# Optimization experiments

Hardware: AMD Instinct MI355X
Metric: run time of the kernel (lower is better)

Reference implementation:

```python
import jax, jax.numpy as jnp
import numpy as np

HIDDEN = 1024
MEM = 50
MAX_POS = 200
BATCH, SEQ = 256, 200


def setup_inputs() -> dict:
    key = jax.random.key(0)
    ks = jax.random.split(key, 5)
    x = jax.random.normal(ks[0], (BATCH, SEQ, HIDDEN), dtype=jnp.float32)
    spatial_memory = jax.random.normal(ks[1], (MEM, HIDDEN), dtype=jnp.float32)
    pos_encoding = jax.random.normal(ks[2], (1, MAX_POS, HIDDEN), dtype=jnp.float32)
    # nn.Linear(2H, H): weight [H, 2H], bias [H]
    bound = 1.0 / np.sqrt(2 * HIDDEN)
    gate_w = jax.random.uniform(ks[3], (HIDDEN, 2 * HIDDEN), jnp.float32, -bound, bound)
    gate_b = jax.random.uniform(ks[4], (HIDDEN,), jnp.float32, -bound, bound)
    return {"x": x, "spatial_memory": spatial_memory, "pos_encoding": pos_encoding,
            "gate_w": gate_w, "gate_b": gate_b}


def reference(x, spatial_memory, pos_encoding, gate_w, gate_b):
    seq_len = x.shape[1]
    # add position encoding (sliced to seq_len)
    feats = x + pos_encoding[:, :seq_len, :]                      # [B,S,H]
    # cross-attention over small fixed memory bank
    sim = jnp.einsum('bsh,mh->bsm', feats, spatial_memory)        # [B,S,M]
    w = jax.nn.softmax(sim, axis=-1)
    mem_read = jnp.einsum('bsm,mh->bsh', w, spatial_memory)       # [B,S,H]
    # gated update: sigmoid(Linear(concat)) -- split weight to avoid concat
    w_f, w_m = gate_w[:, :HIDDEN], gate_w[:, HIDDEN:]
    gate = jax.nn.sigmoid(jnp.einsum('bsh,oh->bso', feats, w_f)
                          + jnp.einsum('bsh,oh->bso', mem_read, w_m)
                          + gate_b)
    return feats + gate * mem_read
```

## Files before the change

kernel.cpp:

```cpp
#include <hip/hip_runtime.h>
#include <cstdint>
#include <cstddef>

#define HD   1024
#define SEQL 200
#define MEMN 50
#define RTOT 51200
#define KP   128
#define PADK 136

typedef float  f4    __attribute__((ext_vector_type(4)));
typedef float  f32x4 __attribute__((ext_vector_type(4)));
typedef short  s16x8 __attribute__((ext_vector_type(8)));
typedef unsigned short u16;
typedef unsigned short u16x4 __attribute__((ext_vector_type(4)));
typedef unsigned short u16x8 __attribute__((ext_vector_type(8)));

__device__ __forceinline__ u16 f2bf(float f) {
    unsigned u = __builtin_bit_cast(unsigned, f);
    u += 0x7FFFu + ((u >> 16) & 1u);
    return (u16)(u >> 16);
}
__device__ __forceinline__ float bf2f(u16 h) {
    unsigned u = ((unsigned)h) << 16;
    return __builtin_bit_cast(float, u);
}

#define GLOAD_LDS16(g, l) __builtin_amdgcn_global_load_lds( \
    (const __attribute__((address_space(1))) unsigned int*)(g), \
    (__attribute__((address_space(3))) unsigned int*)(l), 16, 0, 0)

#define WAITV3 asm volatile("s_waitcnt vmcnt(3)" ::: "memory")
#define WAITV0 asm volatile("s_waitcnt vmcnt(0)" ::: "memory")
#define LGKMFENCE asm volatile("s_waitcnt lgkmcnt(0)" ::: "memory")
#define SCHB   __builtin_amdgcn_sched_barrier(0)

__global__ __launch_bounds__(256) void k_cvt_w(const float* __restrict__ gw,
                                               u16* __restrict__ gwB)
{
    const size_t i = ((size_t)blockIdx.x * 256 + threadIdx.x) * 8;
    f4 v0 = *(const f4*)&gw[i];
    f4 v1 = *(const f4*)&gw[i + 4];
    u16x4 b0 = { f2bf(v0.x), f2bf(v0.y), f2bf(v0.z), f2bf(v0.w) };
    u16x4 b1 = { f2bf(v1.x), f2bf(v1.y), f2bf(v1.z), f2bf(v1.w) };
    *(u16x4*)&gwB[i]     = b0;
    *(u16x4*)&gwB[i + 4] = b1;
}

__global__ __launch_bounds__(256) void k_prep_mem(const float* __restrict__ sm,
                                                  u16* __restrict__ memHi,
                                                  u16* __restrict__ memLo,
                                                  u16* __restrict__ memT)
{
    const int idx = blockIdx.x * 256 + threadIdx.x;
    const int m  = idx >> 8;
    const int h0 = (idx & 255) * 4;
    f4 v = {0.f, 0.f, 0.f, 0.f};
    if (m < MEMN) v = *(const f4*)&sm[(size_t)m * HD + h0];
    u16x4 hi = { f2bf(v.x), f2bf(v.y), f2bf(v.z), f2bf(v.w) };
    f4 hv = { bf2f(hi.x), bf2f(hi.y), bf2f(hi.z), bf2f(hi.w) };
    f4 lv = v - hv;
    u16x4 lo = { f2bf(lv.x), f2bf(lv.y), f2bf(lv.z), f2bf(lv.w) };
    *(u16x4*)&memHi[(size_t)m * HD + h0] = hi;
    *(u16x4*)&memLo[(size_t)m * HD + h0] = lo;
    memT[(size_t)(h0 + 0) * 64 + m] = hi.x;
    memT[(size_t)(h0 + 1) * 64 + m] = hi.y;
    memT[(size_t)(h0 + 2) * 64 + m] = hi.z;
    memT[(size_t)(h0 + 3) * 64 + m] = hi.w;
}

__global__ __launch_bounds__(256) void k_mwm(const u16* __restrict__ memHi,
                                             const u16* __restrict__ gwB,
                                             u16* __restrict__ MWmT)
{
    const int tid = threadIdx.x, lane = tid & 63, w = tid >> 6;
    const int fr = lane & 15, fk = (lane >> 4) * 8, jr = (lane >> 4) * 4;
    const int ob = blockIdx.x * 64 + w * 16;
    f32x4 acc[4] = {};
    for (int ks = 0; ks < 32; ++ks) {
        s16x8 b = *(const s16x8*)&gwB[(size_t)(ob + fr) * 2048 + 1024 + ks * 32 + fk];
        #pragma unroll
        for (int mt = 0; mt < 4; ++mt) {
            s16x8 a = *(const s16x8*)&memHi[(size_t)(mt * 16 + fr) * HD + ks * 32 + fk];
            acc[mt] = __builtin_amdgcn_mfma_f32_16x16x32_bf16(a, b, acc[mt], 0, 0, 0);
        }
    }
    #pragma unroll
    for (int mt = 0; mt < 4; ++mt)
        #pragma unroll
        for (int j = 0; j < 4; ++j)
            MWmT[(size_t)(ob + fr) * 64 + mt * 16 + jr + j] = f2bf(acc[mt][j]);
}

__global__ __launch_bounds__(256) void k_pre(
    const float* __restrict__ x, const float* __restrict__ pos,
    const u16* __restrict__ memHi, const u16* __restrict__ memLo,
    u16* __restrict__ featsB, u16* __restrict__ wBg)
{
    __shared__ u16 fHi[64 * PADK];
    __shared__ u16 fLo[64 * PADK];

    const int tid  = threadIdx.x;
    const int r0   = blockIdx.x * 64;
    const int lane = tid & 63, w = tid >> 6;
    const int fr   = lane & 15;
    const int fk   = (lane >> 4) * 8;
    const int jr   = (lane >> 4) * 4;

    const int srow = tid >> 2;
    const int scol = (tid & 3) * 8;
    const int prow = (r0 + srow) % SEQL;

    const float* xrow = &x[(size_t)(r0 + srow) * HD];
    const float* prp  = &pos[(size_t)prow * HD];

    f4 xa[4][2], pa[4][2];
    #pragma unroll
    for (int i = 0; i < 4; ++i) {
        const int c = scol + i * 32;
        xa[i][0] = *(const f4*)&xrow[c];
        xa[i][1] = *(const f4*)&xrow[c + 4];
        pa[i][0] = *(const f4*)&prp[c];
        pa[i][1] = *(const f4*)&prp[c + 4];
    }

    f32x4 acc[4] = {};

    for (int kp = 0; kp < HD; kp += KP) {
        #pragma unroll
        for (int i = 0; i < 4; ++i) {
            const int c = scol + i * 32;
            f4 fa = xa[i][0] + pa[i][0];
            f4 fb = xa[i][1] + pa[i][1];
            u16x8 hi = { f2bf(fa.x), f2bf(fa.y), f2bf(fa.z), f2bf(fa.w),
                         f2bf(fb.x), f2bf(fb.y), f2bf(fb.z), f2bf(fb.w) };
            *(u16x8*)&featsB[(size_t)(r0 + srow) * HD + kp + c] = hi;
            f4 hv0 = { bf2f(hi[0]), bf2f(hi[1]), bf2f(hi[2]), bf2f(hi[3]) };
            f4 hv1 = { bf2f(hi[4]), bf2f(hi[5]), bf2f(hi[6]), bf2f(hi[7]) };
            f4 l0 = fa - hv0, l1 = fb - hv1;
            u16x8 lo = { f2bf(l0.x), f2bf(l0.y), f2bf(l0.z), f2bf(l0.w),
                         f2bf(l1.x), f2bf(l1.y), f2bf(l1.z), f2bf(l1.w) };
            *(u16x8*)&fHi[srow * PADK + c] = hi;
            *(u16x8*)&fLo[srow * PADK + c] = lo;
        }
        LGKMFENCE;

        if (kp + KP < HD) {
            #pragma unroll
            for (int i = 0; i < 4; ++i) {
                const int c = kp + KP + scol + i * 32;
                xa[i][0] = *(const f4*)&xrow[c];
                xa[i][1] = *(const f4*)&xrow[c + 4];
                pa[i][0] = *(const f4*)&prp[c];
                pa[i][1] = *(const f4*)&prp[c + 4];
            }
        }

        #pragma unroll
        for (int ks = 0; ks < KP / 32; ++ks) {
            const int kb = ks * 32 + fk;
            s16x8 aH = *(const s16x8*)&fHi[(16 * w + fr) * PADK + kb];
            s16x8 aL = *(const s16x8*)&fLo[(16 * w + fr) * PADK + kb];
            #pragma unroll
            for (int n = 0; n < 4; ++n) {
                const size_t mb = (size_t)(n * 16 + fr) * HD + kp + kb;
                s16x8 bH = *(const s16x8*)&memHi[mb];
                s16x8 bL = *(const s16x8*)&memLo[mb];
                acc[n] = __builtin_amdgcn_mfma_f32_16x16x32_bf16(aH, bH, acc[n], 0, 0, 0);
                acc[n] = __builtin_amdgcn_mfma_f32_16x16x32_bf16(aH, bL, acc[n], 0, 0, 0);
                acc[n] = __builtin_amdgcn_mfma_f32_16x16x32_bf16(aL, bH, acc[n], 0, 0, 0);
            }
        }
        LGKMFENCE;
    }

    #pragma unroll
    for (int j = 0; j < 4; ++j) {
        const int rg = r0 + 16 * w + jr + j;
        float v[4];
        float mx = -1e30f;
        #pragma unroll
        for (int n = 0; n < 4; ++n) {
            v[n] = acc[n][j];
            const int m = n * 16 + fr;
            if (m < MEMN) mx = fmaxf(mx, v[n]);
        }
        #pragma unroll
        for (int d = 1; d < 16; d <<= 1) mx = fmaxf(mx, __shfl_xor(mx, d));
        float e[4], s = 0.f;
        #pragma unroll
        for (int n = 0; n < 4; ++n) {
            const int m = n * 16 + fr;
            e[n] = (m < MEMN) ? __expf(v[n] - mx) : 0.f;
            s += e[n];
        }
        #pragma unroll
        for (int d = 1; d < 16; d <<= 1) s += __shfl_xor(s, d);
        const float inv = 1.f / s;
        #pragma unroll
        for (int n = 0; n < 4; ++n)
            wBg[(size_t)rg * 64 + n * 16 + fr] = f2bf(e[n] * inv);
    }
}

__global__ __launch_bounds__(512) void k_gate_out(
    const u16* __restrict__ featsB, const u16* __restrict__ wBg,
    const u16* __restrict__ gwB, const u16* __restrict__ memT,
    const u16* __restrict__ MWmT, const float* __restrict__ gb,
    float* __restrict__ out)
{
    __shared__ u16 As[2][256 * 32];
    __shared__ u16 Bs[2][128 * 32];

    const int tid = threadIdx.x;
    int bid = blockIdx.x;
    bid = (bid & 7) * 200 + (bid >> 3);
    const int mt = bid >> 3, nt = bid & 7;
    const int row0 = mt * 256, col0 = nt * 128;
    const int lane = tid & 63, wave = tid >> 6;
    const int wm = wave >> 1, wn = wave & 1;
    const int fr = lane & 15, fk = (lane >> 4) * 8;

    f32x4 acc[4][4] = {};

    const int sr = tid >> 2;
    const int sc = (tid & 3) * 8;

    auto stage = [&](int buf, int kt) {
        if (kt < 32) {
            const int k0 = kt * 32;
            GLOAD_LDS16(featsB + (size_t)(row0 + sr) * HD + k0 + sc,       &As[buf][tid * 8]);
            GLOAD_LDS16(featsB + (size_t)(row0 + 128 + sr) * HD + k0 + sc, &As[buf][4096 + tid * 8]);
            GLOAD_LDS16(gwB + (size_t)(col0 + sr) * 2048 + k0 + sc,        &Bs[buf][tid * 8]);
        } else {
            const int k0 = (kt - 32) * 32;
            GLOAD_LDS16(wBg + (size_t)(row0 + sr) * 64 + k0 + sc,          &As[buf][tid * 8]);
            GLOAD_LDS16(wBg + (size_t)(row0 + 128 + sr) * 64 + k0 + sc,    &As[buf][4096 + tid * 8]);
            GLOAD_LDS16(MWmT + (size_t)(col0 + sr) * 64 + k0 + sc,         &Bs[buf][tid * 8]);
        }
    };

    stage(0, 0);
    int cur = 0;

    for (int kt = 0; kt < 34; ++kt) {
        if (kt < 33) {
            stage(cur ^ 1, kt + 1);
            WAITV3;
        } else {
            WAITV0;
        }
        __builtin_amdgcn_s_barrier();
        SCHB;

        s16x8 aF[4], bF[4];
        #pragma unroll
        for (int m = 0; m < 4; ++m)
            aF[m] = *(const s16x8*)&As[cur][(wm * 64 + m * 16 + fr) * 32 + fk];
        #pragma unroll
        for (int n = 0; n < 4; ++n)
            bF[n] = *(const s16x8*)&Bs[cur][(wn * 64 + n * 16 + fr) * 32 + fk];
        #pragma unroll
        for (int m = 0; m < 4; ++m)
            #pragma unroll
            for (int n = 0; n < 4; ++n)
                acc[m][n] = __builtin_amdgcn_mfma_f32_16x16x32_bf16(
                    aF[m], bF[n], acc[m][n], 0, 0, 0);

        SCHB;
        __builtin_amdgcn_s_barrier();
        cur ^= 1;
    }

    #pragma unroll
    for (int m = 0; m < 4; ++m) {
        const size_t ab = (size_t)(row0 + wm * 64 + m * 16 + fr) * 64 + fk;
        s16x8 a2_0 = *(const s16x8*)&wBg[ab];
        s16x8 a2_1 = *(const s16x8*)&wBg[ab + 32];
        #pragma unroll
        for (int n = 0; n < 4; ++n) {
            const size_t cb = (size_t)(col0 + wn * 64 + n * 16 + fr) * 64 + fk;
            s16x8 bT0 = *(const s16x8*)&memT[cb];
            s16x8 bT1 = *(const s16x8*)&memT[cb + 32];
            f32x4 accR = {};
            accR = __builtin_amdgcn_mfma_f32_16x16x32_bf16(a2_0, bT0, accR, 0, 0, 0);
            accR = __builtin_amdgcn_mfma_f32_16x16x32_bf16(a2_1, bT1, accR, 0, 0, 0);

            const int crow = row0 + wm * 64 + m * 16 + (lane >> 4) * 4;
            const int ccol = col0 + wn * 64 + n * 16 + fr;
            const float bias = gb[ccol];
            #pragma unroll
            for (int j = 0; j < 4; ++j) {
                const size_t idx = (size_t)(crow + j) * HD + ccol;
                const float fe = bf2f(featsB[idx]);
                const float pre = acc[m][n][j] + bias;
                const float g = 1.0f / (1.0f + __expf(-pre));
                out[idx] = fe + g * accR[j];
            }
        }
    }
}

extern "C" void kernel_launch(void* const* d_in, const int* in_sizes, int n_in,
                              void* d_out, int out_size, void* d_ws, size_t ws_size,
                              hipStream_t stream)
{
    const float* x   = (const float*)d_in[0];
    const float* sm  = (const float*)d_in[1];
    const float* pos = (const float*)d_in[2];
    const float* gw  = (const float*)d_in[3];
    const float* gb  = (const float*)d_in[4];
    float* out = (float*)d_out;

    u16* featsB = (u16*)d_ws;
    u16* gwB    = featsB + (size_t)RTOT * HD;
    u16* wBg    = gwB + (size_t)HD * 2048;
    u16* memHi  = wBg + (size_t)RTOT * 64;
    u16* memLo  = memHi + 64 * HD;
    u16* memT   = memLo + 64 * HD;
    u16* MWmT   = memT + (size_t)HD * 64;

    k_cvt_w<<<dim3(1024), dim3(256), 0, stream>>>(gw, gwB);
    k_prep_mem<<<dim3(64), dim3(256), 0, stream>>>(sm, memHi, memLo, memT);
    k_mwm<<<dim3(16), dim3(256), 0, stream>>>(memHi, gwB, MWmT);
    k_pre<<<dim3(RTOT / 64), dim3(256), 0, stream>>>(x, pos, memHi, memLo,
                                                     featsB, wBg);
    k_gate_out<<<dim3(1600), dim3(512), 0, stream>>>(featsB, wBg, gwB, memT,
                                                     MWmT, gb, out);
}
```

Measured before the change: 441.8 us.

## Triple-buffer gate GEMM with BK=64, XOR-swizzled LDS, and split-phase staging

Restructures the main gate GEMM loop: K tile doubles from 32 to 64, LDS goes from double to triple buffering, and staging is split into two chunks interleaved with the two MFMA phases of each tile. LDS rows are XOR-swizzled to avoid bank conflicts on fragment reads, and s_setprio raises wave priority around the MFMA blocks. The aim is deeper prefetch and fewer barriers per K step so global loads hide better behind compute. It raises LDS use to about 144KB per block, and together with the launch_bounds min-blocks hint of 2 this may limit occupancy.

```diff
diff --git a/kernel.cpp b/kernel.cpp
--- a/kernel.cpp
+++ b/kernel.cpp
@@ -30,7 +30,7 @@
     (const __attribute__((address_space(1))) unsigned int*)(g), \
     (__attribute__((address_space(3))) unsigned int*)(l), 16, 0, 0)
 
-#define WAITV3 asm volatile("s_waitcnt vmcnt(3)" ::: "memory")
+#define WAITV6 asm volatile("s_waitcnt vmcnt(6)" ::: "memory")
 #define WAITV0 asm volatile("s_waitcnt vmcnt(0)" ::: "memory")
 #define LGKMFENCE asm volatile("s_waitcnt lgkmcnt(0)" ::: "memory")
 #define SCHB   __builtin_amdgcn_sched_barrier(0)
@@ -203,14 +203,14 @@
     }
 }
 
-__global__ __launch_bounds__(512) void k_gate_out(
+__global__ __launch_bounds__(512, 2) void k_gate_out(
     const u16* __restrict__ featsB, const u16* __restrict__ wBg,
     const u16* __restrict__ gwB, const u16* __restrict__ memT,
     const u16* __restrict__ MWmT, const float* __restrict__ gb,
     float* __restrict__ out)
 {
-    __shared__ u16 As[2][256 * 32];
-    __shared__ u16 Bs[2][128 * 32];
+    __shared__ u16 As[3][256 * 64];
+    __shared__ u16 Bs[3][128 * 64];
 
     const int tid = threadIdx.x;
     int bid = blockIdx.x;
@@ -219,57 +219,83 @@
     const int row0 = mt * 256, col0 = nt * 128;
     const int lane = tid & 63, wave = tid >> 6;
     const int wm = wave >> 1, wn = wave & 1;
-    const int fr = lane & 15, fk = (lane >> 4) * 8;
+    const int fr = lane & 15, sg = lane >> 4;
+    const int fk = sg * 8;
 
     f32x4 acc[4][4] = {};
 
-    const int sr = tid >> 2;
-    const int sc = (tid & 3) * 8;
-
-    auto stage = [&](int buf, int kt) {
-        if (kt < 32) {
-            const int k0 = kt * 32;
-            GLOAD_LDS16(featsB + (size_t)(row0 + sr) * HD + k0 + sc,       &As[buf][tid * 8]);
-            GLOAD_LDS16(featsB + (size_t)(row0 + 128 + sr) * HD + k0 + sc, &As[buf][4096 + tid * 8]);
-            GLOAD_LDS16(gwB + (size_t)(col0 + sr) * 2048 + k0 + sc,        &Bs[buf][tid * 8]);
+    const int rr = tid >> 3;
+    const int sl = tid & 7;
+
+    auto stageChunk = [&](int buf, int kt, int c) {
+        if (kt < 16) {
+            const int k0 = kt * 64;
+            const int ra0 = c * 128 + rr;
+            GLOAD_LDS16(featsB + (size_t)(row0 + ra0) * HD + k0 + ((sl ^ (ra0 & 7)) * 8),
+                        &As[buf][(c * 128) * 64 + tid * 8]);
+            const int ra1 = c * 128 + 64 + rr;
+            GLOAD_LDS16(featsB + (size_t)(row0 + ra1) * HD + k0 + ((sl ^ (ra1 & 7)) * 8),
+                        &As[buf][(c * 128 + 64) * 64 + tid * 8]);
+            const int rb = c * 64 + rr;
+            GLOAD_LDS16(gwB + (size_t)(col0 + rb) * 2048 + k0 + ((sl ^ (rb & 7)) * 8),
+                        &Bs[buf][(c * 64) * 64 + tid * 8]);
         } else {
-            const int k0 = (kt - 32) * 32;
-            GLOAD_LDS16(wBg + (size_t)(row0 + sr) * 64 + k0 + sc,          &As[buf][tid * 8]);
-            GLOAD_LDS16(wBg + (size_t)(row0 + 128 + sr) * 64 + k0 + sc,    &As[buf][4096 + tid * 8]);
-            GLOAD_LDS16(MWmT + (size_t)(col0 + sr) * 64 + k0 + sc,         &Bs[buf][tid * 8]);
+            const int ra0 = c * 128 + rr;
+            GLOAD_LDS16(wBg + (size_t)(row0 + ra0) * 64 + ((sl ^ (ra0 & 7)) * 8),
+                        &As[buf][(c * 128) * 64 + tid * 8]);
+            const int ra1 = c * 128 + 64 + rr;
+            GLOAD_LDS16(wBg + (size_t)(row0 + ra1) * 64 + ((sl ^ (ra1 & 7)) * 8),
+                        &As[buf][(c * 128 + 64) * 64 + tid * 8]);
+            const int rb = c * 64 + rr;
+            GLOAD_LDS16(MWmT + (size_t)(col0 + rb) * 64 + ((sl ^ (rb & 7)) * 8),
+                        &Bs[buf][(c * 64) * 64 + tid * 8]);
         }
     };
 
-    stage(0, 0);
-    int cur = 0;
-
-    for (int kt = 0; kt < 34; ++kt) {
-        if (kt < 33) {
-            stage(cur ^ 1, kt + 1);
-            WAITV3;
-        } else {
-            WAITV0;
-        }
-        __builtin_amdgcn_s_barrier();
-        SCHB;
-
-        s16x8 aF[4], bF[4];
-        #pragma unroll
-        for (int m = 0; m < 4; ++m)
-            aF[m] = *(const s16x8*)&As[cur][(wm * 64 + m * 16 + fr) * 32 + fk];
-        #pragma unroll
-        for (int n = 0; n < 4; ++n)
-            bF[n] = *(const s16x8*)&Bs[cur][(wn * 64 + n * 16 + fr) * 32 + fk];
-        #pragma unroll
-        for (int m = 0; m < 4; ++m)
-            #pragma unroll
-            for (int n = 0; n < 4; ++n)
-                acc[m][n] = __builtin_amdgcn_mfma_f32_16x16x32_bf16(
-                    aF[m], bF[n], acc[m][n], 0, 0, 0);
-
-        SCHB;
-        __builtin_amdgcn_s_barrier();
-        cur ^= 1;
+    stageChunk(0, 0, 0); stageChunk(0, 0, 1);
+    stageChunk(1, 1, 0); stageChunk(1, 1, 1);
+    WAITV6;
+    __builtin_amdgcn_s_barrier();
+
+    s16x8 aF[4], bF[4];
+
+    for (int T = 0; T < 17; ++T) {
+        const int buf = T % 3;
+        const int nbuf = (T + 2) % 3;
+        const bool doStage = (T + 2 <= 16);
+
+        #pragma unroll
+        for (int ph = 0; ph < 2; ++ph) {
+            #pragma unroll
+            for (int i = 0; i < 4; ++i) {
+                const int r = wm * 64 + i * 16 + fr;
+                const int s = (ph * 4 + sg) ^ (fr & 7);
+                aF[i] = *(const s16x8*)&As[buf][r * 64 + s * 8];
+            }
+            #pragma unroll
+            for (int n = 0; n < 4; ++n) {
+                const int r = wn * 64 + n * 16 + fr;
+                const int s = (ph * 4 + sg) ^ (fr & 7);
+                bF[n] = *(const s16x8*)&Bs[buf][r * 64 + s * 8];
+            }
+            if (doStage) stageChunk(nbuf, T + 2, ph);
+            if (ph == 1) {
+                if (T <= 14)      WAITV6;
+                else if (T == 15) WAITV0;
+            }
+            __builtin_amdgcn_s_barrier();
+            LGKMFENCE;
+            SCHB;
+            __builtin_amdgcn_s_setprio(1);
+            #pragma unroll
+            for (int i = 0; i < 4; ++i)
+                #pragma unroll
+                for (int n = 0; n < 4; ++n)
+                    acc[i][n] = __builtin_amdgcn_mfma_f32_16x16x32_bf16(
+                        aF[i], bF[n], acc[i][n], 0, 0, 0);
+            __builtin_amdgcn_s_setprio(0);
+            __builtin_amdgcn_s_barrier();
+        }
     }
 
     #pragma unroll
@@ -286,7 +312,7 @@
             accR = __builtin_amdgcn_mfma_f32_16x16x32_bf16(a2_0, bT0, accR, 0, 0, 0);
             accR = __builtin_amdgcn_mfma_f32_16x16x32_bf16(a2_1, bT1, accR, 0, 0, 0);
 
-            const int crow = row0 + wm * 64 + m * 16 + (lane >> 4) * 4;
+            const int crow = row0 + wm * 64 + m * 16 + sg * 4;
             const int ccol = col0 + wn * 64 + n * 16 + fr;
             const float bias = gb[ccol];
             #pragma unroll
```

New measurement: 444.0 us. Within noise of the previous version (+0.5%).

## Split feature conversion from similarity kernel and stage bf16 tiles via async LDS loads

Applied to the files above, without the earlier changes.

Moves the x+pos add and the bf16 hi/lo split into a separate streaming kernel that writes featsB and a lo-part buffer (placed in the output buffer as scratch). The similarity kernel then double-buffers those bf16 tiles into XOR-swizzled shared memory with global_load_lds and waitcnt fencing, instead of converting in registers with lgkm fences. The aim is to overlap loads with the MFMA work and remove the serialized conversion in the sim loop. The cost is an extra round trip through global memory for the lo buffer (about 100MB written and read back) plus one more kernel launch.

```diff
diff --git a/kernel.cpp b/kernel.cpp
--- a/kernel.cpp
+++ b/kernel.cpp
@@ -6,8 +6,6 @@
 #define SEQL 200
 #define MEMN 50
 #define RTOT 51200
-#define KP   128
-#define PADK 136
 
 typedef float  f4    __attribute__((ext_vector_type(4)));
 typedef float  f32x4 __attribute__((ext_vector_type(4)));
@@ -30,9 +28,9 @@
     (const __attribute__((address_space(1))) unsigned int*)(g), \
     (__attribute__((address_space(3))) unsigned int*)(l), 16, 0, 0)
 
+#define WAITV4 asm volatile("s_waitcnt vmcnt(4)" ::: "memory")
 #define WAITV3 asm volatile("s_waitcnt vmcnt(3)" ::: "memory")
 #define WAITV0 asm volatile("s_waitcnt vmcnt(0)" ::: "memory")
-#define LGKMFENCE asm volatile("s_waitcnt lgkmcnt(0)" ::: "memory")
 #define SCHB   __builtin_amdgcn_sched_barrier(0)
 
 __global__ __launch_bounds__(256) void k_cvt_w(const float* __restrict__ gw,
@@ -92,78 +90,80 @@
             MWmT[(size_t)(ob + fr) * 64 + mt * 16 + jr + j] = f2bf(acc[mt][j]);
 }
 
-__global__ __launch_bounds__(256) void k_pre(
-    const float* __restrict__ x, const float* __restrict__ pos,
+__global__ __launch_bounds__(256) void k_feats(const float* __restrict__ x,
+                                               const float* __restrict__ pos,
+                                               u16* __restrict__ featsB,
+                                               u16* __restrict__ featsLo)
+{
+    const size_t stride = (size_t)gridDim.x * 256 * 8;
+    for (size_t e = ((size_t)blockIdx.x * 256 + threadIdx.x) * 8;
+         e < (size_t)RTOT * HD; e += stride) {
+        const int row  = (int)(e >> 10);
+        const int col  = (int)(e & 1023);
+        const int prow = row % SEQL;
+        f4 x0 = *(const f4*)&x[e];
+        f4 x1 = *(const f4*)&x[e + 4];
+        f4 p0 = *(const f4*)&pos[(size_t)prow * HD + col];
+        f4 p1 = *(const f4*)&pos[(size_t)prow * HD + col + 4];
+        f4 fa = x0 + p0, fb = x1 + p1;
+        u16x8 hi = { f2bf(fa.x), f2bf(fa.y), f2bf(fa.z), f2bf(fa.w),
+                     f2bf(fb.x), f2bf(fb.y), f2bf(fb.z), f2bf(fb.w) };
+        f4 hv0 = { bf2f(hi[0]), bf2f(hi[1]), bf2f(hi[2]), bf2f(hi[3]) };
+        f4 hv1 = { bf2f(hi[4]), bf2f(hi[5]), bf2f(hi[6]), bf2f(hi[7]) };
+        f4 l0 = fa - hv0, l1 = fb - hv1;
+        u16x8 lo = { f2bf(l0.x), f2bf(l0.y), f2bf(l0.z), f2bf(l0.w),
+                     f2bf(l1.x), f2bf(l1.y), f2bf(l1.z), f2bf(l1.w) };
+        *(u16x8*)&featsB[e]  = hi;
+        *(u16x8*)&featsLo[e] = lo;
+    }
+}
+
+__global__ __launch_bounds__(256) void k_sim(
+    const u16* __restrict__ featsB, const u16* __restrict__ featsLo,
     const u16* __restrict__ memHi, const u16* __restrict__ memLo,
-    u16* __restrict__ featsB, u16* __restrict__ wBg)
-{
-    __shared__ u16 fHi[64 * PADK];
-    __shared__ u16 fLo[64 * PADK];
+    u16* __restrict__ wBg)
+{
+    __shared__ u16 S[2][4][2][1024];
 
     const int tid  = threadIdx.x;
+    const int lane = tid & 63, w = tid >> 6;
+    const int fr   = lane & 15, sg = lane >> 4;
+    const int fk   = sg * 8, jr = sg * 4;
     const int r0   = blockIdx.x * 64;
-    const int lane = tid & 63, w = tid >> 6;
-    const int fr   = lane & 15;
-    const int fk   = (lane >> 4) * 8;
-    const int jr   = (lane >> 4) * 4;
-
-    const int srow = tid >> 2;
-    const int scol = (tid & 3) * 8;
-    const int prow = (r0 + srow) % SEQL;
-
-    const float* xrow = &x[(size_t)(r0 + srow) * HD];
-    const float* prp  = &pos[(size_t)prow * HD];
-
-    f4 xa[4][2], pa[4][2];
-    #pragma unroll
-    for (int i = 0; i < 4; ++i) {
-        const int c = scol + i * 32;
-        xa[i][0] = *(const f4*)&xrow[c];
-        xa[i][1] = *(const f4*)&xrow[c + 4];
-        pa[i][0] = *(const f4*)&prp[c];
-        pa[i][1] = *(const f4*)&prp[c + 4];
-    }
+    const int rowbase = r0 + 16 * w;
+
+    const int lrow = lane >> 3;
+    const int lslot = lane & 7;
+    const int srcsl = (lslot ^ lrow) * 8;
+
+    auto stage = [&](int b, int p) {
+        #pragma unroll
+        for (int g = 0; g < 2; ++g) {
+            const int r = rowbase + g * 8 + lrow;
+            GLOAD_LDS16(featsB  + (size_t)r * HD + p * 64 + srcsl,
+                        &S[b][w][0][g * 512]);
+            GLOAD_LDS16(featsLo + (size_t)r * HD + p * 64 + srcsl,
+                        &S[b][w][1][g * 512]);
+        }
+    };
 
     f32x4 acc[4] = {};
 
-    for (int kp = 0; kp < HD; kp += KP) {
-        #pragma unroll
-        for (int i = 0; i < 4; ++i) {
-            const int c = scol + i * 32;
-            f4 fa = xa[i][0] + pa[i][0];
-            f4 fb = xa[i][1] + pa[i][1];
-            u16x8 hi = { f2bf(fa.x), f2bf(fa.y), f2bf(fa.z), f2bf(fa.w),
-                         f2bf(fb.x), f2bf(fb.y), f2bf(fb.z), f2bf(fb.w) };
-            *(u16x8*)&featsB[(size_t)(r0 + srow) * HD + kp + c] = hi;
-            f4 hv0 = { bf2f(hi[0]), bf2f(hi[1]), bf2f(hi[2]), bf2f(hi[3]) };
-            f4 hv1 = { bf2f(hi[4]), bf2f(hi[5]), bf2f(hi[6]), bf2f(hi[7]) };
-            f4 l0 = fa - hv0, l1 = fb - hv1;
-            u16x8 lo = { f2bf(l0.x), f2bf(l0.y), f2bf(l0.z), f2bf(l0.w),
-                         f2bf(l1.x), f2bf(l1.y), f2bf(l1.z), f2bf(l1.w) };
-            *(u16x8*)&fHi[srow * PADK + c] = hi;
-            *(u16x8*)&fLo[srow * PADK + c] = lo;
-        }
-        LGKMFENCE;
-
-        if (kp + KP < HD) {
-            #pragma unroll
-            for (int i = 0; i < 4; ++i) {
-                const int c = kp + KP + scol + i * 32;
-                xa[i][0] = *(const f4*)&xrow[c];
-                xa[i][1] = *(const f4*)&xrow[c + 4];
-                pa[i][0] = *(const f4*)&prp[c];
-                pa[i][1] = *(const f4*)&prp[c + 4];
-            }
-        }
-
-        #pragma unroll
-        for (int ks = 0; ks < KP / 32; ++ks) {
-            const int kb = ks * 32 + fk;
-            s16x8 aH = *(const s16x8*)&fHi[(16 * w + fr) * PADK + kb];
-            s16x8 aL = *(const s16x8*)&fLo[(16 * w + fr) * PADK + kb];
+    stage(0, 0);
+    for (int p = 0; p < 16; ++p) {
+        const int b = p & 1;
+        if (p < 15) { stage(b ^ 1, p + 1); WAITV4; }
+        else        { WAITV0; }
+        SCHB;
+
+        #pragma unroll
+        for (int ks = 0; ks < 2; ++ks) {
+            const int sl = ((ks * 4 + sg) ^ (fr & 7)) * 8;
+            s16x8 aH = *(const s16x8*)&S[b][w][0][fr * 64 + sl];
+            s16x8 aL = *(const s16x8*)&S[b][w][1][fr * 64 + sl];
             #pragma unroll
             for (int n = 0; n < 4; ++n) {
-                const size_t mb = (size_t)(n * 16 + fr) * HD + kp + kb;
+                const size_t mb = (size_t)(n * 16 + fr) * HD + p * 64 + ks * 32 + fk;
                 s16x8 bH = *(const s16x8*)&memHi[mb];
                 s16x8 bL = *(const s16x8*)&memLo[mb];
                 acc[n] = __builtin_amdgcn_mfma_f32_16x16x32_bf16(aH, bH, acc[n], 0, 0, 0);
@@ -171,7 +171,6 @@
                 acc[n] = __builtin_amdgcn_mfma_f32_16x16x32_bf16(aL, bH, acc[n], 0, 0, 0);
             }
         }
-        LGKMFENCE;
     }
 
     #pragma unroll
@@ -320,11 +319,14 @@
     u16* memT   = memLo + 64 * HD;
     u16* MWmT   = memT + (size_t)HD * 64;
 
+    u16* featsLo = (u16*)d_out;
+
     k_cvt_w<<<dim3(1024), dim3(256), 0, stream>>>(gw, gwB);
     k_prep_mem<<<dim3(64), dim3(256), 0, stream>>>(sm, memHi, memLo, memT);
     k_mwm<<<dim3(16), dim3(256), 0, stream>>>(memHi, gwB, MWmT);
-    k_pre<<<dim3(RTOT / 64), dim3(256), 0, stream>>>(x, pos, memHi, memLo,
-                                                     featsB, wBg);
+    k_feats<<<dim3(1600), dim3(256), 0, stream>>>(x, pos, featsB, featsLo);
+    k_sim<<<dim3(RTOT / 64), dim3(256), 0, stream>>>(featsB, featsLo,
+                                                     memHi, memLo, wBg);
     k_gate_out<<<dim3(1600), dim3(512), 0, stream>>>(featsB, wBg, gwB, memT,
                                                      MWmT, gb, out);
 }
```

After: 471.5 us. +6.7%, slower.

## Stage swizzled memory bank through LDS with double-buffered async loads in k_pre

Applied to the files above, without the earlier changes.

Rather than having every wave read the hi/lo memory-bank operands straight from global memory, k_prep_mem now writes them in an XOR-swizzled, panel-major layout. k_pre then copies 64-column panels into double-buffered LDS through direct global-to-LDS loads, overlapped with the feature conversion. The K panel shrinks from 128 to 64 columns, and a workgroup barrier is added each step. The aim is to cut redundant global/L2 traffic and bank conflicts, at the cost of more LDS use and an extra barrier per step. The reuse of a fLo/fHi and memory buffer across iterations relies on that barrier ordering, so a read-write race is a risk.

```diff
diff --git a/kernel.cpp b/kernel.cpp
--- a/kernel.cpp
+++ b/kernel.cpp
@@ -6,8 +6,7 @@
 #define SEQL 200
 #define MEMN 50
 #define RTOT 51200
-#define KP   128
-#define PADK 136
+#define PK   72
 
 typedef float  f4    __attribute__((ext_vector_type(4)));
 typedef float  f32x4 __attribute__((ext_vector_type(4)));
@@ -49,8 +48,9 @@
 
 __global__ __launch_bounds__(256) void k_prep_mem(const float* __restrict__ sm,
                                                   u16* __restrict__ memHi,
-                                                  u16* __restrict__ memLo,
-                                                  u16* __restrict__ memT)
+                                                  u16* __restrict__ memT,
+                                                  u16* __restrict__ memSH,
+                                                  u16* __restrict__ memSL)
 {
     const int idx = blockIdx.x * 256 + threadIdx.x;
     const int m  = idx >> 8;
@@ -62,11 +62,14 @@
     f4 lv = v - hv;
     u16x4 lo = { f2bf(lv.x), f2bf(lv.y), f2bf(lv.z), f2bf(lv.w) };
     *(u16x4*)&memHi[(size_t)m * HD + h0] = hi;
-    *(u16x4*)&memLo[(size_t)m * HD + h0] = lo;
     memT[(size_t)(h0 + 0) * 64 + m] = hi.x;
     memT[(size_t)(h0 + 1) * 64 + m] = hi.y;
     memT[(size_t)(h0 + 2) * 64 + m] = hi.z;
     memT[(size_t)(h0 + 3) * 64 + m] = hi.w;
+    const int p = h0 >> 6, s = (h0 >> 3) & 7, e = h0 & 7;
+    const size_t sw = (size_t)p * 4096 + m * 64 + ((s ^ (m & 7)) << 3) + e;
+    *(u16x4*)&memSH[sw] = hi;
+    *(u16x4*)&memSL[sw] = lo;
 }
 
 __global__ __launch_bounds__(256) void k_mwm(const u16* __restrict__ memHi,
@@ -94,84 +97,98 @@
 
 __global__ __launch_bounds__(256) void k_pre(
     const float* __restrict__ x, const float* __restrict__ pos,
-    const u16* __restrict__ memHi, const u16* __restrict__ memLo,
+    const u16* __restrict__ memSH, const u16* __restrict__ memSL,
     u16* __restrict__ featsB, u16* __restrict__ wBg)
 {
-    __shared__ u16 fHi[64 * PADK];
-    __shared__ u16 fLo[64 * PADK];
+    __shared__ u16 fHi[64 * PK];
+    __shared__ u16 fLo[64 * PK];
+    __shared__ u16 memH[2][64 * 64];
+    __shared__ u16 memL[2][64 * 64];
 
     const int tid  = threadIdx.x;
     const int r0   = blockIdx.x * 64;
     const int lane = tid & 63, w = tid >> 6;
-    const int fr   = lane & 15;
-    const int fk   = (lane >> 4) * 8;
-    const int jr   = (lane >> 4) * 4;
+    const int fr   = lane & 15, sg = lane >> 4;
+    const int fk   = sg * 8, jr = sg * 4;
 
     const int srow = tid >> 2;
-    const int scol = (tid & 3) * 8;
+    const int scol = (tid & 3) * 16;
     const int prow = (r0 + srow) % SEQL;
-
     const float* xrow = &x[(size_t)(r0 + srow) * HD];
     const float* prp  = &pos[(size_t)prow * HD];
 
-    f4 xa[4][2], pa[4][2];
+    f4 xa[4], pa[4];
     #pragma unroll
     for (int i = 0; i < 4; ++i) {
-        const int c = scol + i * 32;
-        xa[i][0] = *(const f4*)&xrow[c];
-        xa[i][1] = *(const f4*)&xrow[c + 4];
-        pa[i][0] = *(const f4*)&prp[c];
-        pa[i][1] = *(const f4*)&prp[c + 4];
-    }
+        xa[i] = *(const f4*)&xrow[scol + i * 4];
+        pa[i] = *(const f4*)&prp[scol + i * 4];
+    }
+    GLOAD_LDS16(memSH + tid * 8,        &memH[0][tid * 8]);
+    GLOAD_LDS16(memSH + 2048 + tid * 8, &memH[0][2048 + tid * 8]);
+    GLOAD_LDS16(memSL + tid * 8,        &memL[0][tid * 8]);
+    GLOAD_LDS16(memSL + 2048 + tid * 8, &memL[0][2048 + tid * 8]);
 
     f32x4 acc[4] = {};
 
-    for (int kp = 0; kp < HD; kp += KP) {
-        #pragma unroll
-        for (int i = 0; i < 4; ++i) {
-            const int c = scol + i * 32;
-            f4 fa = xa[i][0] + pa[i][0];
-            f4 fb = xa[i][1] + pa[i][1];
-            u16x8 hi = { f2bf(fa.x), f2bf(fa.y), f2bf(fa.z), f2bf(fa.w),
-                         f2bf(fb.x), f2bf(fb.y), f2bf(fb.z), f2bf(fb.w) };
-            *(u16x8*)&featsB[(size_t)(r0 + srow) * HD + kp + c] = hi;
-            f4 hv0 = { bf2f(hi[0]), bf2f(hi[1]), bf2f(hi[2]), bf2f(hi[3]) };
-            f4 hv1 = { bf2f(hi[4]), bf2f(hi[5]), bf2f(hi[6]), bf2f(hi[7]) };
-            f4 l0 = fa - hv0, l1 = fb - hv1;
-            u16x8 lo = { f2bf(l0.x), f2bf(l0.y), f2bf(l0.z), f2bf(l0.w),
-                         f2bf(l1.x), f2bf(l1.y), f2bf(l1.z), f2bf(l1.w) };
-            *(u16x8*)&fHi[srow * PADK + c] = hi;
-            *(u16x8*)&fLo[srow * PADK + c] = lo;
+    for (int p = 0; p < 16; ++p) {
+        const int b = p & 1;
+        WAITV0;
+
+        {
+            f4 f0 = xa[0] + pa[0], f1 = xa[1] + pa[1];
+            f4 f2 = xa[2] + pa[2], f3 = xa[3] + pa[3];
+            u16x8 h0 = { f2bf(f0.x), f2bf(f0.y), f2bf(f0.z), f2bf(f0.w),
+                         f2bf(f1.x), f2bf(f1.y), f2bf(f1.z), f2bf(f1.w) };
+            u16x8 h1 = { f2bf(f2.x), f2bf(f2.y), f2bf(f2.z), f2bf(f2.w),
+                         f2bf(f3.x), f2bf(f3.y), f2bf(f3.z), f2bf(f3.w) };
+            *(u16x8*)&featsB[(size_t)(r0 + srow) * HD + p * 64 + scol]     = h0;
+            *(u16x8*)&featsB[(size_t)(r0 + srow) * HD + p * 64 + scol + 8] = h1;
+            f4 hv0 = { bf2f(h0[0]), bf2f(h0[1]), bf2f(h0[2]), bf2f(h0[3]) };
+            f4 hv1 = { bf2f(h0[4]), bf2f(h0[5]), bf2f(h0[6]), bf2f(h0[7]) };
+            f4 hv2 = { bf2f(h1[0]), bf2f(h1[1]), bf2f(h1[2]), bf2f(h1[3]) };
+            f4 hv3 = { bf2f(h1[4]), bf2f(h1[5]), bf2f(h1[6]), bf2f(h1[7]) };
+            f4 l0 = f0 - hv0, l1 = f1 - hv1, l2 = f2 - hv2, l3 = f3 - hv3;
+            u16x8 lo0 = { f2bf(l0.x), f2bf(l0.y), f2bf(l0.z), f2bf(l0.w),
+                          f2bf(l1.x), f2bf(l1.y), f2bf(l1.z), f2bf(l1.w) };
+            u16x8 lo1 = { f2bf(l2.x), f2bf(l2.y), f2bf(l2.z), f2bf(l2.w),
+                          f2bf(l3.x), f2bf(l3.y), f2bf(l3.z), f2bf(l3.w) };
+            *(u16x8*)&fHi[srow * PK + scol]     = h0;
+            *(u16x8*)&fHi[srow * PK + scol + 8] = h1;
+            *(u16x8*)&fLo[srow * PK + scol]     = lo0;
+            *(u16x8*)&fLo[srow * PK + scol + 8] = lo1;
         }
         LGKMFENCE;
-
-        if (kp + KP < HD) {
+        __builtin_amdgcn_s_barrier();
+
+        if (p < 15) {
+            const size_t mo = (size_t)(p + 1) * 4096;
+            GLOAD_LDS16(memSH + mo + tid * 8,        &memH[b ^ 1][tid * 8]);
+            GLOAD_LDS16(memSH + mo + 2048 + tid * 8, &memH[b ^ 1][2048 + tid * 8]);
+            GLOAD_LDS16(memSL + mo + tid * 8,        &memL[b ^ 1][tid * 8]);
+            GLOAD_LDS16(memSL + mo + 2048 + tid * 8, &memL[b ^ 1][2048 + tid * 8]);
+            const int c = (p + 1) * 64 + scol;
             #pragma unroll
             for (int i = 0; i < 4; ++i) {
-                const int c = kp + KP + scol + i * 32;
-                xa[i][0] = *(const f4*)&xrow[c];
-                xa[i][1] = *(const f4*)&xrow[c + 4];
-                pa[i][0] = *(const f4*)&prp[c];
-                pa[i][1] = *(const f4*)&prp[c + 4];
+                xa[i] = *(const f4*)&xrow[c + i * 4];
+                pa[i] = *(const f4*)&prp[c + i * 4];
             }
         }
 
         #pragma unroll
-        for (int ks = 0; ks < KP / 32; ++ks) {
-            const int kb = ks * 32 + fk;
-            s16x8 aH = *(const s16x8*)&fHi[(16 * w + fr) * PADK + kb];
-            s16x8 aL = *(const s16x8*)&fLo[(16 * w + fr) * PADK + kb];
+        for (int ks = 0; ks < 2; ++ks) {
+            s16x8 aH = *(const s16x8*)&fHi[(16 * w + fr) * PK + ks * 32 + fk];
+            s16x8 aL = *(const s16x8*)&fLo[(16 * w + fr) * PK + ks * 32 + fk];
             #pragma unroll
             for (int n = 0; n < 4; ++n) {
-                const size_t mb = (size_t)(n * 16 + fr) * HD + kp + kb;
-                s16x8 bH = *(const s16x8*)&memHi[mb];
-                s16x8 bL = *(const s16x8*)&memLo[mb];
+                const int m = n * 16 + fr;
+                const int slot = ((ks * 4 + sg) ^ (m & 7)) * 8;
+                s16x8 bH = *(const s16x8*)&memH[b][m * 64 + slot];
+                s16x8 bL = *(const s16x8*)&memL[b][m * 64 + slot];
                 acc[n] = __builtin_amdgcn_mfma_f32_16x16x32_bf16(aH, bH, acc[n], 0, 0, 0);
                 acc[n] = __builtin_amdgcn_mfma_f32_16x16x32_bf16(aH, bL, acc[n], 0, 0, 0);
                 acc[n] = __builtin_amdgcn_mfma_f32_16x16x32_bf16(aL, bH, acc[n], 0, 0, 0);
             }
         }
-        LGKMFENCE;
     }
 
     #pragma unroll
@@ -316,14 +333,15 @@
     u16* gwB    = featsB + (size_t)RTOT * HD;
     u16* wBg    = gwB + (size_t)HD * 2048;
     u16* memHi  = wBg + (size_t)RTOT * 64;
-    u16* memLo  = memHi + 64 * HD;
-    u16* memT   = memLo + 64 * HD;
+    u16* memT   = memHi + 64 * HD;
     u16* MWmT   = memT + (size_t)HD * 64;
+    u16* memSH  = MWmT + (size_t)HD * 64;
+    u16* memSL  = memSH + (size_t)64 * HD;
 
     k_cvt_w<<<dim3(1024), dim3(256), 0, stream>>>(gw, gwB);
-    k_prep_mem<<<dim3(64), dim3(256), 0, stream>>>(sm, memHi, memLo, memT);
+    k_prep_mem<<<dim3(64), dim3(256), 0, stream>>>(sm, memHi, memT, memSH, memSL);
     k_mwm<<<dim3(16), dim3(256), 0, stream>>>(memHi, gwB, MWmT);
-    k_pre<<<dim3(RTOT / 64), dim3(256), 0, stream>>>(x, pos, memHi, memLo,
+    k_pre<<<dim3(RTOT / 64), dim3(256), 0, stream>>>(x, pos, memSH, memSL,
                                                      featsB, wBg);
     k_gate_out<<<dim3(1600), dim3(512), 0, stream>>>(featsB, wBg, gwB, memT,
                                                      MWmT, gb, out);
```

After: 370.0 us (median of 2 runs). 1.19x faster.
